# Performance work log

Measured on AMD Instinct MI355X. Metric: run time of the kernel, lower is better.

Reference implementation:

```python
import jax, jax.numpy as jnp
import numpy as np

N, E = 20000, 320000
IN_DIM = OUT_DIM = E_IN = E_OUT = 128
BN_EPS = 1e-5

def _lrelu(x):
    return jnp.where(x >= 0, x, 0.1 * x)

def setup_inputs() -> dict:
    key = jax.random.key(0)
    ks = jax.random.split(key, 12)
    def w(k, shape):
        return jax.random.normal(k, shape, jnp.float32) * (shape[0] ** -0.5)
    return {
        "h": jax.random.normal(ks[0], (N, IN_DIM), jnp.float32),
        "edge_w": jax.random.normal(ks[1], (E, E_IN), jnp.float32),
        "W_node": w(ks[2], (IN_DIM, OUT_DIM)),
        "W_eedge": w(ks[3], (E_IN, E_IN)),
        "W_esf": w(ks[4], (E_IN, 1)),
        "W_fuse": w(ks[5], (2 * OUT_DIM + E_IN, OUT_DIM)),
        "b_fuse": jnp.zeros((OUT_DIM,), jnp.float32),
        "W_attn": w(ks[6], (OUT_DIM, 1)),
        "W_conc": w(ks[7], (2 * OUT_DIM + E_IN, OUT_DIM)),
        "b_conc": jnp.zeros((OUT_DIM,), jnp.float32),
        "bn_gamma": jnp.ones((E_IN,), jnp.float32),
        "bn_beta": jnp.zeros((E_IN,), jnp.float32),
        "W_aggre": w(ks[8], (2 * OUT_DIM + 2 * E_IN, E_OUT)),
        "src": jax.random.randint(ks[9], (E,), 0, N),
        "dst": jax.random.randint(ks[10], (E,), 0, N),
    }

def reference(h, edge_w, W_node, W_eedge, W_esf, W_fuse, b_fuse, W_attn,
              W_conc, b_conc, bn_gamma, bn_beta, W_aggre, src, dst):
    # eval mode: dropout = identity, BatchNorm uses running stats (mean 0, var 1)
    hn = h @ W_node                       # embed_node -> ndata['h'] = ndata['oh']
    # self_attention: ow = embed_edge(w); w = edge_sf_atten(lrelu(ow)) * ow
    ow = edge_w @ W_eedge                 # [E, e_in]
    w1 = (_lrelu(ow) @ W_esf) * ow        # [E, e_in]
    # inter_attention
    hs, hd = hn[src], hn[dst]             # [E, out]
    sat = jnp.concatenate([hs, hd, w1], axis=-1)          # [E, 2*out+e_in]
    inw = _lrelu(sat @ W_fuse + b_fuse)                   # [E, out]
    a = inw @ W_attn                                      # [E, 1]
    w2 = a * w1                                           # edata['w']
    # reduce_func2: segment softmax over incoming edges (grouped by dst)
    s = a[:, 0]
    m = jax.ops.segment_max(s, dst, num_segments=N)
    e = jnp.exp(s - m[dst])
    denom = jax.ops.segment_sum(e, dst, num_segments=N)
    alpha = (e / denom[dst])[:, None]                     # [E, 1]
    t = jnp.concatenate([hs, w2], axis=-1)                # [E, out+e_in]
    h_agg = jax.ops.segment_sum(alpha * t, dst, num_segments=N)  # [N, out+e_in]
    h_new = jnp.concatenate([h_agg, hn], axis=-1) @ W_conc + b_conc
    # DGL only updates nodes that received messages; zero-indegree keep embed_node(h)
    indeg = jax.ops.segment_sum(jnp.ones((E,), jnp.float32), dst, num_segments=N)
    h_out = jnp.where(indeg[:, None] > 0, h_new, hn)      # [N, out]
    # edge_calc: BN(w2) then aggre_embed_edge(cat(src_h, dst_h, bn_w, ow))
    w_bn = (w2 / jnp.sqrt(jnp.float32(1.0) + BN_EPS)) * bn_gamma + bn_beta
    z = jnp.concatenate([h_out[src], h_out[dst], w_bn, ow], axis=-1)
    w_out = z @ W_aggre                                   # [E, e_out]
    return h_out, w_out, sat
```

## Files before the change

### kernel.cpp

```cpp
#include <hip/hip_runtime.h>
#include <hip/hip_bf16.h>

#define TB 256
#define TBM 512
#define BM 64
#define BK 32
#define BN 128
#define ASTR 68
#define MAXD 160

static constexpr int NN = 20000;
static constexpr int NE = 320000;

static constexpr long long OFF_HN   = 0;
static constexpr long long OFF_OW   = 2560000;
static constexpr long long OFF_S    = 43520000;
static constexpr long long OFF_DEN  = 43840000;
static constexpr long long OFF_CUR  = 43860000;
static constexpr long long OFF_HAGG = 43880000;
static constexpr long long OFF_WT   = 49000000;
static constexpr long long WS_FLOATS = 49140000;

static constexpr int U_E = 0;
static constexpr int U_F = 32768;
static constexpr int U_A = 131072;

static constexpr long long OUT_HOUT = 0;
static constexpr long long OUT_WOUT = 2560000;
static constexpr long long OUT_SAT  = 43520000;

typedef __attribute__((ext_vector_type(8))) short s8v;
typedef __attribute__((ext_vector_type(4))) float f32x4;
typedef __attribute__((ext_vector_type(4))) unsigned short u16x4;

#define MFMA16(a,b,c) __builtin_amdgcn_mfma_f32_16x16x32_bf16(a,b,c,0,0,0)

__device__ __forceinline__ float lrelu(float x){ return x >= 0.f ? x : 0.1f*x; }

__device__ __forceinline__ void gl16(const void* g, void* l){
    __builtin_amdgcn_global_load_lds(
        (const __attribute__((address_space(1))) void*)g,
        (__attribute__((address_space(3))) void*)l, 16, 0, 0);
}

__device__ __forceinline__ void split1(float f, unsigned short& hi, unsigned short& lo){
    __hip_bfloat16 h = __float2bfloat16(f);
    float hf = __bfloat162float(h);
    __hip_bfloat16 l = __float2bfloat16(f - hf);
    hi = __builtin_bit_cast(unsigned short, h);
    lo = __builtin_bit_cast(unsigned short, l);
}
__device__ __forceinline__ void split8(float4 a, float4 b, s8v& hi, s8v& lo){
    float v[8] = {a.x,a.y,a.z,a.w,b.x,b.y,b.z,b.w};
#pragma unroll
    for (int j = 0; j < 8; ++j){
        unsigned short hs, ls;
        split1(v[j], hs, ls);
        hi[j] = (short)hs; lo[j] = (short)ls;
    }
}
__device__ __forceinline__ float bfp(unsigned p){
    return __uint_as_float(p & 0xffff0000u) + __uint_as_float(p << 16);
}

__device__ __forceinline__ int lds_a(int row, int g){
    return row*32 + ((g ^ (row & 3)) << 3);
}

__device__ __forceinline__ void store_At(float (*Ast)[ASTR], int k4, int r, float4 v){
    Ast[k4+0][r] = v.x; Ast[k4+1][r] = v.y; Ast[k4+2][r] = v.z; Ast[k4+3][r] = v.w;
}
__device__ __forceinline__ void mm_chunk(const float (*Ast)[ASTR], const float (*Bs)[BN],
                                         int r0, int c0, float acc[4][8]){
#pragma unroll 4
    for (int k = 0; k < BK; ++k){
        const float4 av = *(const float4*)&Ast[k][r0];
        const float4 b0 = *(const float4*)&Bs[k][c0];
        const float4 b1 = *(const float4*)&Bs[k][64 + c0];
        const float a0=av.x, a1=av.y, a2=av.z, a3=av.w;
        const float b[8] = {b0.x,b0.y,b0.z,b0.w,b1.x,b1.y,b1.z,b1.w};
#pragma unroll
        for (int j = 0; j < 8; ++j){
            acc[0][j] = fmaf(a0, b[j], acc[0][j]);
            acc[1][j] = fmaf(a1, b[j], acc[1][j]);
            acc[2][j] = fmaf(a2, b[j], acc[2][j]);
            acc[3][j] = fmaf(a3, b[j], acc[3][j]);
        }
    }
}
__device__ __forceinline__ void load_B(const float* __restrict__ W, int kc,
                                       float (*Bs)[BN], int tid){
#pragma unroll
    for (int p = 0; p < 4; ++p){
        int idx = p*TB + tid;
        int row = idx >> 5;
        int c4  = (idx & 31) << 2;
        *(float4*)&Bs[row][c4] = *(const float4*)&W[(size_t)(kc+row)*BN + c4];
    }
}

__global__ __launch_bounds__(TB) void k_prep(const float* __restrict__ We,
                                             const float* __restrict__ Wf,
                                             const float* __restrict__ Wa,
                                             unsigned short* __restrict__ wt,
                                             int* __restrict__ cur){
    int id = blockIdx.x*TB + threadIdx.x;
    if (id < NN) cur[id] = 0;
    unsigned short hs, ls;
    if (id < 16384){
        int n = id >> 7, k = id & 127;
        split1(We[(size_t)k*128 + n], hs, ls);
        wt[U_E + id] = hs; wt[U_E + 16384 + id] = ls;
    } else if (id < 65536){
        int local = id - 16384;
        int n = local / 384, k = local - n*384;
        split1(Wf[(size_t)k*128 + n], hs, ls);
        wt[U_F + local] = hs; wt[U_F + 49152 + local] = ls;
    } else if (id < 131072){
        int local = id - 65536;
        int n = local >> 9, k = local & 511;
        split1(Wa[(size_t)k*128 + n], hs, ls);
        wt[U_A + local] = hs; wt[U_A + 65536 + local] = ls;
    }
}

__global__ __launch_bounds__(TB) void kB_count(const int* __restrict__ dst,
                                               int* __restrict__ cur){
    int e = blockIdx.x*TB + threadIdx.x;
    atomicAdd(&cur[dst[e]], 1);
}
__global__ __launch_bounds__(TB) void kC_scan(int* __restrict__ cur,
                                              int* __restrict__ offs){
    __shared__ int part[TB];
    __shared__ int spre[TB];
    const int tid = threadIdx.x;
    const int CH = (NN + TB - 1) / TB;
    const int base = tid * CH;
    int sum = 0;
    for (int i = 0; i < CH; ++i){ int idx = base + i; if (idx < NN) sum += cur[idx]; }
    part[tid] = sum;
    __syncthreads();
    if (tid == 0){ int r = 0; for (int i = 0; i < TB; ++i){ spre[i] = r; r += part[i]; } }
    __syncthreads();
    int run = spre[tid];
    for (int i = 0; i < CH; ++i){
        int idx = base + i;
        if (idx < NN){ int c = cur[idx]; offs[idx] = run; cur[idx] = run; run += c; }
    }
}
__global__ __launch_bounds__(TB) void kD_scatter(const int* __restrict__ dst,
                                                 int* __restrict__ cur,
                                                 int* __restrict__ eidx){
    int e = blockIdx.x*TB + threadIdx.x;
    int p = atomicAdd(&cur[dst[e]], 1);
    eidx[p] = e;
}

__global__ __launch_bounds__(TB) void k1_hn(const float* __restrict__ h,
                                            const float* __restrict__ Wn,
                                            unsigned short* __restrict__ hnH,
                                            unsigned short* __restrict__ hnL,
                                            unsigned* __restrict__ hnP){
    __shared__ float Ast[BK][ASTR];
    __shared__ float Bs[BK][BN];
    const int tid = threadIdx.x;
    const int rbase = blockIdx.x * BM;
    const int tc = tid & 15, tr = tid >> 4;
    const int r0 = tr*4, c0 = tc*4;
    float acc[4][8] = {};
    for (int kc = 0; kc < 128; kc += BK){
        __syncthreads();
        {
            int lr = tid >> 3, k4 = (tid & 7) << 2;
#pragma unroll
            for (int p = 0; p < 2; ++p){
                int r = p*32 + lr;
                int rr = rbase + r; if (rr >= NN) rr = NN-1;
                float4 v = *(const float4*)&h[(size_t)rr*128 + kc + k4];
                store_At(Ast, k4, r, v);
            }
        }
        load_B(Wn, kc, Bs, tid);
        __syncthreads();
        mm_chunk(Ast, Bs, r0, c0, acc);
    }
#pragma unroll
    for (int i = 0; i < 4; ++i){
        int rr = rbase + r0 + i;
        if (rr < NN){
            u16x4 h0, l0, h1, l1;
            uint4 p0, p1;
#pragma unroll
            for (int j = 0; j < 4; ++j){
                unsigned short hs, ls;
                split1(acc[i][j], hs, ls);
                h0[j] = hs; l0[j] = ls;
                ((unsigned*)&p0)[j] = ((unsigned)hs << 16) | ls;
                split1(acc[i][4+j], hs, ls);
                h1[j] = hs; l1[j] = ls;
                ((unsigned*)&p1)[j] = ((unsigned)hs << 16) | ls;
            }
            *(u16x4*)&hnH[(size_t)rr*128 + c0] = h0;
            *(u16x4*)&hnL[(size_t)rr*128 + c0] = l0;
            *(u16x4*)&hnH[(size_t)rr*128 + 64 + c0] = h1;
            *(u16x4*)&hnL[(size_t)rr*128 + 64 + c0] = l1;
            *(uint4*)&hnP[(size_t)rr*128 + c0] = p0;
            *(uint4*)&hnP[(size_t)rr*128 + 64 + c0] = p1;
        }
    }
}


__global__ __launch_bounds__(TBM) void k2_mfma(const float* __restrict__ ew,
                                               const unsigned short* __restrict__ wtH,
                                               const unsigned short* __restrict__ wtL,
                                               const float* __restrict__ Wesf,
                                               unsigned short* __restrict__ owH,
                                               unsigned short* __restrict__ owL,
                                               float* __restrict__ sat){
    __shared__ __align__(16) unsigned short Ah[2][4096], Al[2][4096], Bh[2][4096], Bl[2][4096];
    __shared__ float sEsf[128];
    const int tid = threadIdx.x;
    const long long rbase = (long long)blockIdx.x * 128;
    const int lane = tid & 63, w = tid >> 6;
    const int ls = lane & 15, lg = lane >> 4;
    const int srow = tid >> 2, sg = tid & 3;
    const int gsw = sg ^ (srow & 3);
    const int aslot = srow*32 + (gsw << 3);
    if (tid < 128) sEsf[tid] = Wesf[tid];
    f32x4 acc[8] = {};
    auto stage = [&](int nb, int t){
        const int kc = t*32;
        gl16(&wtH[srow*128 + kc + gsw*8], &Bh[nb][w*512]);
        gl16(&wtL[srow*128 + kc + gsw*8], &Bl[nb][w*512]);
        const float* p = &ew[(rbase + srow)*128 + kc + sg*8];
        float4 v0 = *(const float4*)p, v1 = *(const float4*)(p+4);
        s8v hi, lo; split8(v0, v1, hi, lo);
        *(s8v*)&Ah[nb][aslot] = hi; *(s8v*)&Al[nb][aslot] = lo;
    };
    stage(0, 0);
    __syncthreads();
    int cur = 0;
    for (int t = 0; t < 4; ++t){
        if (t+1 < 4) stage(cur^1, t+1);
        s8v ah = *(const s8v*)&Ah[cur][lds_a(w*16 + ls, lg)];
        s8v al = *(const s8v*)&Al[cur][lds_a(w*16 + ls, lg)];
#pragma unroll
        for (int ct = 0; ct < 8; ++ct){
            int c = ct*16 + ls;
            s8v bh = *(const s8v*)&Bh[cur][lds_a(c,lg)];
            s8v bl = *(const s8v*)&Bl[cur][lds_a(c,lg)];
            acc[ct] = MFMA16(ah, bh, acc[ct]);
            acc[ct] = MFMA16(ah, bl, acc[ct]);
            acc[ct] = MFMA16(al, bh, acc[ct]);
        }
        __syncthreads();
        cur ^= 1;
    }
#pragma unroll
    for (int reg = 0; reg < 4; ++reg){
        float p = 0.f;
#pragma unroll
        for (int ct = 0; ct < 8; ++ct)
            p += lrelu(acc[ct][reg]) * sEsf[ct*16 + ls];
#pragma unroll
        for (int m = 1; m < 16; m <<= 1) p += __shfl_xor(p, m);
        long long orow = rbase + w*16 + lg*4 + reg;
#pragma unroll
        for (int ct = 0; ct < 8; ++ct){
            float o = acc[ct][reg];
            int col = ct*16 + ls;
            sat[orow*384 + 256 + col] = p * o;
            unsigned short hs_, ls_; split1(o, hs_, ls_);
            owH[orow*128 + col] = hs_;
            owL[orow*128 + col] = ls_;
        }
    }
}

__global__ __launch_bounds__(TBM) void k3_mfma(const unsigned short* __restrict__ hnH,
                                               const unsigned short* __restrict__ hnL,
                                               const unsigned* __restrict__ hnP,
                                               const unsigned short* __restrict__ wtH,
                                               const unsigned short* __restrict__ wtL,
                                               const float* __restrict__ bf,
                                               const float* __restrict__ Wattn,
                                               const int* __restrict__ src,
                                               const int* __restrict__ dst,
                                               float* __restrict__ sat,
                                               float* __restrict__ s_ws){
    __shared__ __align__(16) unsigned short Ah[2][4096], Al[2][4096], Bh[2][4096], Bl[2][4096];
    __shared__ float sBf[128], sAtt[128];
    __shared__ int sSrc[128], sDst[128];
    const int tid = threadIdx.x;
    const long long rbase = (long long)blockIdx.x * 128;
    const int lane = tid & 63, w = tid >> 6;
    const int ls = lane & 15, lg = lane >> 4;
    const int srow = tid >> 2, sg = tid & 3;
    const int gsw = sg ^ (srow & 3);
    const int aslot = srow*32 + (gsw << 3);
    if (tid < 128){
        sBf[tid] = bf[tid]; sAtt[tid] = Wattn[tid];
        sSrc[tid] = src[rbase + tid]; sDst[tid] = dst[rbase + tid];
    }
    __syncthreads();
    f32x4 acc[8] = {};
    auto stage = [&](int nb, int t){
        const int kc = t*32;
        gl16(&wtH[srow*384 + kc + gsw*8], &Bh[nb][w*512]);
        gl16(&wtL[srow*384 + kc + gsw*8], &Bl[nb][w*512]);
        long long e = rbase + srow;
        if (kc < 256){
            int node = (kc < 128) ? sSrc[srow] : sDst[srow];
            int col0 = kc & 127;
            gl16(&hnH[(size_t)node*128 + col0 + gsw*8], &Ah[nb][w*512]);
            gl16(&hnL[(size_t)node*128 + col0 + gsw*8], &Al[nb][w*512]);
            const unsigned* pp = &hnP[(size_t)node*128 + col0 + sg*8];
            uint4 q0 = *(const uint4*)pp, q1 = *(const uint4*)(pp+4);
            float4 v0 = {bfp(q0.x), bfp(q0.y), bfp(q0.z), bfp(q0.w)};
            float4 v1 = {bfp(q1.x), bfp(q1.y), bfp(q1.z), bfp(q1.w)};
            *(float4*)&sat[e*384 + kc + sg*8] = v0;
            *(float4*)&sat[e*384 + kc + sg*8 + 4] = v1;
        } else {
            const float* p = &sat[e*384 + kc + sg*8];
            float4 v0 = *(const float4*)p, v1 = *(const float4*)(p+4);
            s8v hi, lo; split8(v0, v1, hi, lo);
            *(s8v*)&Ah[nb][aslot] = hi; *(s8v*)&Al[nb][aslot] = lo;
        }
    };
    stage(0, 0);
    __syncthreads();
    int cur = 0;
    for (int t = 0; t < 12; ++t){
        if (t+1 < 12) stage(cur^1, t+1);
        s8v ah = *(const s8v*)&Ah[cur][lds_a(w*16 + ls, lg)];
        s8v al = *(const s8v*)&Al[cur][lds_a(w*16 + ls, lg)];
#pragma unroll
        for (int ct = 0; ct < 8; ++ct){
            int c = ct*16 + ls;
            s8v bh = *(const s8v*)&Bh[cur][lds_a(c,lg)];
            s8v bl = *(const s8v*)&Bl[cur][lds_a(c,lg)];
            acc[ct] = MFMA16(ah, bh, acc[ct]);
            acc[ct] = MFMA16(ah, bl, acc[ct]);
            acc[ct] = MFMA16(al, bh, acc[ct]);
        }
        __syncthreads();
        cur ^= 1;
    }
#pragma unroll
    for (int reg = 0; reg < 4; ++reg){
        float p = 0.f;
#pragma unroll
        for (int ct = 0; ct < 8; ++ct){
            int col = ct*16 + ls;
            p += lrelu(acc[ct][reg] + sBf[col]) * sAtt[col];
        }
#pragma unroll
        for (int m = 1; m < 16; m <<= 1) p += __shfl_xor(p, m);
        if (ls == 0) s_ws[rbase + w*16 + lg*4 + reg] = p;
    }
}

__global__ __launch_bounds__(TB) void k5_agg(const float* __restrict__ s,
                                             const unsigned* __restrict__ hnP,
                                             const float* __restrict__ sat,
                                             const int* __restrict__ src,
                                             const int* __restrict__ eidx,
                                             const int* __restrict__ offs,
                                             const int* __restrict__ cur,
                                             float* __restrict__ hagg,
                                             float* __restrict__ den){
    __shared__ int   sEu[4][MAXD];
    __shared__ int   sEs[4][MAXD];
    __shared__ float sAl[4][MAXD];
    __shared__ float sWc[4][MAXD];
    const int wv = threadIdx.x >> 6, lane = threadIdx.x & 63;
    const int n = blockIdx.x*4 + wv;
    int* Eu = sEu[wv]; int* Es = sEs[wv];
    float* Al = sAl[wv]; float* Wc = sWc[wv];
    const int start = offs[n];
    const int deg = cur[n] - start;
    const int dc = deg < MAXD ? deg : MAXD;
    for (int i = lane; i < dc; i += 64) Eu[i] = eidx[start+i];
    __syncthreads();
    for (int i = lane; i < dc; i += 64){
        int my = Eu[i], r = 0;
        for (int j = 0; j < dc; ++j) r += (Eu[j] < my);
        Es[r] = my;
    }
    __syncthreads();
    float lm = -3.402823466e38f;
    for (int i = lane; i < dc; i += 64){
        int e = Es[i];
        float sv = s[e];
        Wc[i] = sv;
        Eu[i] = src[e];
        lm = fmaxf(lm, sv);
    }
    for (int i = MAXD + lane; i < deg; i += 64) lm = fmaxf(lm, s[eidx[start+i]]);
#pragma unroll
    for (int m2 = 32; m2; m2 >>= 1) lm = fmaxf(lm, __shfl_xor(lm, m2));
    const float m = lm;
    float lsum = 0.f;
    for (int i = lane; i < dc; i += 64){
        float ev = expf(Wc[i] - m);
        Al[i] = ev;
        lsum += ev;
    }
    for (int i = MAXD + lane; i < deg; i += 64) lsum += expf(s[eidx[start+i]] - m);
#pragma unroll
    for (int m2 = 32; m2; m2 >>= 1) lsum += __shfl_xor(lsum, m2);
    const float denom = lsum;
    const float inv = (deg > 0) ? 1.f/denom : 0.f;
    for (int i = lane; i < dc; i += 64){
        float al = Al[i] * inv;
        Al[i] = al;
        Wc[i] = al * Wc[i];
    }
    __syncthreads();
    float a0=0.f, a1=0.f, a2=0.f, a3=0.f;
    for (int i = 0; i < dc; ++i){
        int sI = Eu[i];
        size_t e = (size_t)Es[i];
        float al = Al[i], wc = Wc[i];
        unsigned p0 = hnP[(size_t)sI*128 + lane];
        unsigned p1 = hnP[(size_t)sI*128 + 64 + lane];
        float w0 = sat[e*384 + 256 + lane];
        float w1v = sat[e*384 + 256 + 64 + lane];
        a0 = fmaf(al, bfp(p0), a0);
        a1 = fmaf(al, bfp(p1), a1);
        a2 = fmaf(wc, w0, a2);
        a3 = fmaf(wc, w1v, a3);
    }
    for (int i = MAXD; i < deg; ++i){
        int e = eidx[start+i];
        float sv = s[e];
        float al = expf(sv - m) * inv;
        float wc = al * sv;
        int sI = src[e];
        a0 = fmaf(al, bfp(hnP[(size_t)sI*128 + lane]), a0);
        a1 = fmaf(al, bfp(hnP[(size_t)sI*128 + 64 + lane]), a1);
        a2 = fmaf(wc, sat[(size_t)e*384 + 256 + lane], a2);
        a3 = fmaf(wc, sat[(size_t)e*384 + 256 + 64 + lane], a3);
    }
    const size_t b = (size_t)n*256;
    hagg[b + lane] = a0;
    hagg[b + 64 + lane] = a1;
    hagg[b + 128 + lane] = a2;
    hagg[b + 192 + lane] = a3;
    if (lane == 0) den[n] = (deg > 0) ? denom : 0.f;
}

__global__ __launch_bounds__(TB) void k6_conc(const float* hagg,
                                              const unsigned* __restrict__ hnP,
                                              const float* __restrict__ Wc,
                                              const float* __restrict__ bc,
                                              const float* __restrict__ den,
                                              float* __restrict__ hout,
                                              unsigned short* houtHL){
    __shared__ float Ast[BK][ASTR];
    __shared__ float Bs[BK][BN];
    __shared__ float sBc[BN];
    const int tid = threadIdx.x;
    const int rbase = blockIdx.x * BM;
    const int tc = tid & 15, tr = tid >> 4;
    const int r0 = tr*4, c0 = tc*4;
    if (tid < BN) sBc[tid] = bc[tid];
    float acc[4][8] = {};
    for (int chunk = 0; chunk < 12; ++chunk){
        int kc = chunk * BK;
        __syncthreads();
        {
            int lr = tid >> 3, k4 = (tid & 7) << 2;
#pragma unroll
            for (int p = 0; p < 2; ++p){
                int r = p*32 + lr;
                int rr = rbase + r; if (rr >= NN) rr = NN-1;
                float4 v;
                if (chunk < 8) v = *(const float4*)&hagg[(size_t)rr*256 + kc + k4];
                else {
                    int cb = (kc - 256) + k4;
                    uint4 q = *(const uint4*)&hnP[(size_t)rr*128 + cb];
                    v.x = bfp(q.x); v.y = bfp(q.y); v.z = bfp(q.z); v.w = bfp(q.w);
                }
                store_At(Ast, k4, r, v);
            }
        }
        load_B(Wc, kc, Bs, tid);
        __syncthreads();
        mm_chunk(Ast, Bs, r0, c0, acc);
    }
#pragma unroll
    for (int i = 0; i < 4; ++i){
        int rr = rbase + r0 + i;
        if (rr >= NN) continue;
        bool keep = den[rr] > 0.f;
        float o[8];
#pragma unroll
        for (int j = 0; j < 8; ++j){
            int col = (j < 4) ? (c0 + j) : (60 + c0 + j);
            float fb = bfp(hnP[(size_t)rr*128 + col]);
            o[j] = keep ? acc[i][j] + sBc[col] : fb;
        }
        float4 o0 = {o[0],o[1],o[2],o[3]}, o1 = {o[4],o[5],o[6],o[7]};
        *(float4*)&hout[(size_t)rr*128 + c0] = o0;
        *(float4*)&hout[(size_t)rr*128 + 64 + c0] = o1;
        u16x4 h0, l0, h1, l1;
#pragma unroll
        for (int j = 0; j < 4; ++j){
            unsigned short hs, ls2;
            split1(o[j], hs, ls2);   h0[j] = hs; l0[j] = ls2;
            split1(o[4+j], hs, ls2); h1[j] = hs; l1[j] = ls2;
        }
        *(u16x4*)&houtHL[(size_t)rr*512 + c0] = h0;
        *(u16x4*)&houtHL[(size_t)rr*512 + 128 + c0] = l0;
        *(u16x4*)&houtHL[(size_t)rr*512 + 64 + c0] = h1;
        *(u16x4*)&houtHL[(size_t)rr*512 + 128 + 64 + c0] = l1;
    }
}

__global__ __launch_bounds__(TBM) void k7_mfma(const unsigned short* __restrict__ houtHL,
                                               const unsigned short* __restrict__ owH,
                                               const unsigned short* __restrict__ owL,
                                               const float* __restrict__ sarr,
                                               const float* __restrict__ sat,
                                               const float* __restrict__ gamma,
                                               const float* __restrict__ beta,
                                               const unsigned short* __restrict__ wtH,
                                               const unsigned short* __restrict__ wtL,
                                               const int* __restrict__ src,
                                               const int* __restrict__ dst,
                                               float* __restrict__ w2out){
    __shared__ __align__(16) unsigned short Ah[2][4096], Al[2][4096], Bh[2][4096], Bl[2][4096];
    __shared__ float sGam[128], sBet[128], sS[128];
    __shared__ int sSrc[128], sDst[128];
    const int tid = threadIdx.x;
    const long long rbase = (long long)blockIdx.x * 128;
    const int lane = tid & 63, w = tid >> 6;
    const int ls = lane & 15, lg = lane >> 4;
    const int srow = tid >> 2, sg = tid & 3;
    const int gsw = sg ^ (srow & 3);
    const int aslot = srow*32 + (gsw << 3);
    const float ISR = 0.9999950000374997f;
    if (tid < 128){
        sGam[tid] = gamma[tid] * ISR; sBet[tid] = beta[tid];
        sSrc[tid] = src[rbase + tid]; sDst[tid] = dst[rbase + tid];
        sS[tid] = sarr[rbase + tid];
    }
    __syncthreads();
    f32x4 acc[8] = {};
    auto stage = [&](int nb, int t){
        const int kc = t*32;
        gl16(&wtH[srow*512 + kc + gsw*8], &Bh[nb][w*512]);
        gl16(&wtL[srow*512 + kc + gsw*8], &Bl[nb][w*512]);
        long long e = rbase + srow;
        if (kc < 256){
            int node = (kc < 128) ? sSrc[srow] : sDst[srow];
            int col0 = kc & 127;
            gl16(&houtHL[(size_t)node*512 + col0 + gsw*8], &Ah[nb][w*512]);
            gl16(&houtHL[(size_t)node*512 + 128 + col0 + gsw*8], &Al[nb][w*512]);
        } else if (kc < 384){
            int cb = (kc - 256) + sg*8;
            float se = sS[srow];
            const float* p = &sat[e*384 + 256 + cb];
            float4 v0 = *(const float4*)p, v1 = *(const float4*)(p+4);
            v0.x = fmaf(v0.x*se, sGam[cb+0], sBet[cb+0]);
            v0.y = fmaf(v0.y*se, sGam[cb+1], sBet[cb+1]);
            v0.z = fmaf(v0.z*se, sGam[cb+2], sBet[cb+2]);
            v0.w = fmaf(v0.w*se, sGam[cb+3], sBet[cb+3]);
            v1.x = fmaf(v1.x*se, sGam[cb+4], sBet[cb+4]);
            v1.y = fmaf(v1.y*se, sGam[cb+5], sBet[cb+5]);
            v1.z = fmaf(v1.z*se, sGam[cb+6], sBet[cb+6]);
            v1.w = fmaf(v1.w*se, sGam[cb+7], sBet[cb+7]);
            s8v hi, lo; split8(v0, v1, hi, lo);
            *(s8v*)&Ah[nb][aslot] = hi; *(s8v*)&Al[nb][aslot] = lo;
        } else {
            int col0 = kc - 384;
            gl16(&owH[e*128 + col0 + gsw*8], &Ah[nb][w*512]);
            gl16(&owL[e*128 + col0 + gsw*8], &Al[nb][w*512]);
        }
    };
    stage(0, 0);
    __syncthreads();
    int cur = 0;
    for (int t = 0; t < 16; ++t){
        if (t+1 < 16) stage(cur^1, t+1);
        s8v ah = *(const s8v*)&Ah[cur][lds_a(w*16 + ls, lg)];
        s8v al = *(const s8v*)&Al[cur][lds_a(w*16 + ls, lg)];
#pragma unroll
        for (int ct = 0; ct < 8; ++ct){
            int c = ct*16 + ls;
            s8v bh = *(const s8v*)&Bh[cur][lds_a(c,lg)];
            s8v bl = *(const s8v*)&Bl[cur][lds_a(c,lg)];
            acc[ct] = MFMA16(ah, bh, acc[ct]);
            acc[ct] = MFMA16(ah, bl, acc[ct]);
            acc[ct] = MFMA16(al, bh, acc[ct]);
        }
        __syncthreads();
        cur ^= 1;
    }
#pragma unroll
    for (int reg = 0; reg < 4; ++reg){
        long long orow = rbase + w*16 + lg*4 + reg;
#pragma unroll
        for (int ct = 0; ct < 8; ++ct)
            w2out[orow*128 + ct*16 + ls] = acc[ct][reg];
    }
}

extern "C" void kernel_launch(void* const* d_in, const int* in_sizes, int n_in,
                              void* d_out, int out_size, void* d_ws, size_t ws_size,
                              hipStream_t stream){
    (void)in_sizes; (void)n_in; (void)out_size;
    const float* h       = (const float*)d_in[0];
    const float* edge_w  = (const float*)d_in[1];
    const float* W_node  = (const float*)d_in[2];
    const float* W_eedge = (const float*)d_in[3];
    const float* W_esf   = (const float*)d_in[4];
    const float* W_fuse  = (const float*)d_in[5];
    const float* b_fuse  = (const float*)d_in[6];
    const float* W_attn  = (const float*)d_in[7];
    const float* W_conc  = (const float*)d_in[8];
    const float* b_conc  = (const float*)d_in[9];
    const float* gamma   = (const float*)d_in[10];
    const float* beta    = (const float*)d_in[11];
    const float* W_aggre = (const float*)d_in[12];
    const int*   src     = (const int*)d_in[13];
    const int*   dst     = (const int*)d_in[14];

    float* out    = (float*)d_out;
    float* o_hout = out + OUT_HOUT;
    float* o_wout = out + OUT_WOUT;
    float* o_sat  = out + OUT_SAT;

    if (ws_size < (size_t)WS_FLOATS * 4) return;
    float* ws     = (float*)d_ws;
    unsigned short* w_hnH = (unsigned short*)(ws + OFF_HN);
    unsigned short* w_hnL = w_hnH + (size_t)NN*128;
    unsigned short* w_owH = (unsigned short*)(ws + OFF_OW);
    unsigned short* w_owL = w_owH + (size_t)NE*128;
    float* w_s    = ws + OFF_S;
    float* w_den  = ws + OFF_DEN;
    int*   w_cur  = (int*)(ws + OFF_CUR);
    float* w_hagg = ws + OFF_HAGG;
    unsigned short* w_houtHL = (unsigned short*)w_hagg;
    unsigned short* w_wt = (unsigned short*)(ws + OFF_WT);

    unsigned* w_hnP = (unsigned*)o_wout;
    int* w_eidx = (int*)o_hout;
    int* w_offs = w_eidx + NE;

    hipLaunchKernelGGL(k_prep,    dim3(131072/TB), dim3(TB), 0, stream,
                       W_eedge, W_fuse, W_aggre, w_wt, w_cur);
    hipLaunchKernelGGL(kB_count,  dim3(NE/TB), dim3(TB), 0, stream, dst, w_cur);
    hipLaunchKernelGGL(kC_scan,   dim3(1), dim3(TB), 0, stream, w_cur, w_offs);
    hipLaunchKernelGGL(kD_scatter,dim3(NE/TB), dim3(TB), 0, stream, dst, w_cur, w_eidx);
    hipLaunchKernelGGL(k1_hn,     dim3((NN+BM-1)/BM), dim3(TB), 0, stream, h, W_node,
                       w_hnH, w_hnL, w_hnP);
    hipLaunchKernelGGL(k2_mfma,   dim3(NE/128), dim3(TBM), 0, stream, edge_w,
                       w_wt + U_E, w_wt + U_E + 128*128, W_esf,
                       w_owH, w_owL, o_sat);
    hipLaunchKernelGGL(k3_mfma,   dim3(NE/128), dim3(TBM), 0, stream, w_hnH, w_hnL, w_hnP,
                       w_wt + U_F, w_wt + U_F + 128*384, b_fuse, W_attn,
                       src, dst, o_sat, w_s);
    hipLaunchKernelGGL(k5_agg,    dim3(NN/4), dim3(TB), 0, stream, w_s, w_hnP, o_sat,
                       src, w_eidx, w_offs, w_cur, w_hagg, w_den);
    hipLaunchKernelGGL(k6_conc,   dim3((NN+BM-1)/BM), dim3(TB), 0, stream, w_hagg,
                       w_hnP, W_conc, b_conc, w_den, o_hout, w_houtHL);
    hipLaunchKernelGGL(k7_mfma,   dim3(NE/128), dim3(TBM), 0, stream, w_houtHL,
                       w_owH, w_owL, w_s, o_sat, gamma, beta,
                       w_wt + U_A, w_wt + U_A + 128*512,
                       src, dst, o_wout);
}
```

Baseline: 711.5 us.

## Precompute per-node projections of h_out through W_aggre instead of per-edge GEMM

The h_out[src] and h_out[dst] slices of the final edge GEMM are moved to node level. A new fp32 kernel computes h_out @ W_aggre rows 0..255 for each of the 20000 nodes, and the edge kernel now runs only K=256 (bn_w and ow) with split-bf16 MFMA. It then adds two gathered 128-wide node rows per edge in the epilogue. This halves the K-loop of the dominant edge GEMM and removes the hi/lo split of h_out. The cost is an extra node GEMM and scattered fp32 gathers of the node projections per edge.

```diff
diff --git a/kernel.cpp b/kernel.cpp
--- a/kernel.cpp
+++ b/kernel.cpp
@@ -11,19 +11,23 @@
 
 static constexpr int NN = 20000;
 static constexpr int NE = 320000;
-
-static constexpr long long OFF_HN   = 0;
-static constexpr long long OFF_OW   = 2560000;
-static constexpr long long OFF_S    = 43520000;
-static constexpr long long OFF_DEN  = 43840000;
-static constexpr long long OFF_CUR  = 43860000;
-static constexpr long long OFF_HAGG = 43880000;
-static constexpr long long OFF_WT   = 49000000;
-static constexpr long long WS_FLOATS = 49140000;
-
-static constexpr int U_E = 0;
-static constexpr int U_F = 32768;
-static constexpr int U_A = 131072;
+static constexpr int NB = 313;
+
+static constexpr long long OFF_OW  = 0;
+static constexpr long long OFF_HN  = 40960000;
+static constexpr long long OFF_PQ  = 43520000;
+static constexpr long long OFF_S   = 48640000;
+static constexpr long long OFF_DEN = 48960000;
+static constexpr long long OFF_CUR = 48980000;
+static constexpr long long OFF_WT  = 49000000;
+static constexpr long long WS_FLOATS = 49100000;
+
+static constexpr int U_EH = 0;
+static constexpr int U_EL = 16384;
+static constexpr int U_FH = 32768;
+static constexpr int U_FL = 81920;
+static constexpr int U_AH = 131072;
+static constexpr int U_AL = 163840;
 
 static constexpr long long OUT_HOUT = 0;
 static constexpr long long OUT_WOUT = 2560000;
@@ -31,6 +35,7 @@
 
 typedef __attribute__((ext_vector_type(8))) short s8v;
 typedef __attribute__((ext_vector_type(4))) float f32x4;
+typedef __attribute__((ext_vector_type(8))) unsigned short u16x8;
 typedef __attribute__((ext_vector_type(4))) unsigned short u16x4;
 
 #define MFMA16(a,b,c) __builtin_amdgcn_mfma_f32_16x16x32_bf16(a,b,c,0,0,0)
@@ -110,17 +115,17 @@
     if (id < 16384){
         int n = id >> 7, k = id & 127;
         split1(We[(size_t)k*128 + n], hs, ls);
-        wt[U_E + id] = hs; wt[U_E + 16384 + id] = ls;
+        wt[U_EH + id] = hs; wt[U_EL + id] = ls;
     } else if (id < 65536){
         int local = id - 16384;
         int n = local / 384, k = local - n*384;
         split1(Wf[(size_t)k*128 + n], hs, ls);
-        wt[U_F + local] = hs; wt[U_F + 49152 + local] = ls;
-    } else if (id < 131072){
+        wt[U_FH + local] = hs; wt[U_FL + local] = ls;
+    } else if (id < 98304){
         int local = id - 65536;
-        int n = local >> 9, k = local & 511;
-        split1(Wa[(size_t)k*128 + n], hs, ls);
-        wt[U_A + local] = hs; wt[U_A + 65536 + local] = ls;
+        int n = local >> 8, kk = local & 255;
+        split1(Wa[(size_t)(256+kk)*128 + n], hs, ls);
+        wt[U_AH + local] = hs; wt[U_AL + local] = ls;
     }
 }
 
@@ -451,13 +456,12 @@
     if (lane == 0) den[n] = (deg > 0) ? denom : 0.f;
 }
 
-__global__ __launch_bounds__(TB) void k6_conc(const float* hagg,
+__global__ __launch_bounds__(TB) void k6_conc(const float* __restrict__ hagg,
                                               const unsigned* __restrict__ hnP,
                                               const float* __restrict__ Wc,
                                               const float* __restrict__ bc,
                                               const float* __restrict__ den,
-                                              float* __restrict__ hout,
-                                              unsigned short* houtHL){
+                                              float* __restrict__ hout){
     __shared__ float Ast[BK][ASTR];
     __shared__ float Bs[BK][BN];
     __shared__ float sBc[BN];
@@ -505,32 +509,61 @@
         float4 o0 = {o[0],o[1],o[2],o[3]}, o1 = {o[4],o[5],o[6],o[7]};
         *(float4*)&hout[(size_t)rr*128 + c0] = o0;
         *(float4*)&hout[(size_t)rr*128 + 64 + c0] = o1;
-        u16x4 h0, l0, h1, l1;
-#pragma unroll
-        for (int j = 0; j < 4; ++j){
-            unsigned short hs, ls2;
-            split1(o[j], hs, ls2);   h0[j] = hs; l0[j] = ls2;
-            split1(o[4+j], hs, ls2); h1[j] = hs; l1[j] = ls2;
-        }
-        *(u16x4*)&houtHL[(size_t)rr*512 + c0] = h0;
-        *(u16x4*)&houtHL[(size_t)rr*512 + 128 + c0] = l0;
-        *(u16x4*)&houtHL[(size_t)rr*512 + 64 + c0] = h1;
-        *(u16x4*)&houtHL[(size_t)rr*512 + 128 + 64 + c0] = l1;
-    }
-}
-
-__global__ __launch_bounds__(TBM) void k7_mfma(const unsigned short* __restrict__ houtHL,
-                                               const unsigned short* __restrict__ owH,
-                                               const unsigned short* __restrict__ owL,
-                                               const float* __restrict__ sarr,
-                                               const float* __restrict__ sat,
-                                               const float* __restrict__ gamma,
-                                               const float* __restrict__ beta,
-                                               const unsigned short* __restrict__ wtH,
-                                               const unsigned short* __restrict__ wtL,
-                                               const int* __restrict__ src,
-                                               const int* __restrict__ dst,
-                                               float* __restrict__ w2out){
+    }
+}
+
+__global__ __launch_bounds__(TB) void kNG(const float* __restrict__ aF,
+                                          const float* __restrict__ W,
+                                          float* __restrict__ O){
+    __shared__ float Ast[BK][ASTR];
+    __shared__ float Bs[BK][BN];
+    const int tid = threadIdx.x;
+    const int half = blockIdx.x >= NB ? 1 : 0;
+    const int rbase = (blockIdx.x - half*NB) * BM;
+    const float* Wp = W + (size_t)half*16384;
+    const int tc = tid & 15, tr = tid >> 4;
+    const int r0 = tr*4, c0 = tc*4;
+    float acc[4][8] = {};
+    for (int kc = 0; kc < 128; kc += BK){
+        __syncthreads();
+        {
+            int lr = tid >> 3, k4 = (tid & 7) << 2;
+#pragma unroll
+            for (int p = 0; p < 2; ++p){
+                int r = p*32 + lr;
+                int rr = rbase + r; if (rr >= NN) rr = NN-1;
+                float4 v = *(const float4*)&aF[(size_t)rr*128 + kc + k4];
+                store_At(Ast, k4, r, v);
+            }
+        }
+        load_B(Wp, kc, Bs, tid);
+        __syncthreads();
+        mm_chunk(Ast, Bs, r0, c0, acc);
+    }
+#pragma unroll
+    for (int i = 0; i < 4; ++i){
+        int rr = rbase + r0 + i;
+        if (rr < NN){
+            float4 o0 = {acc[i][0],acc[i][1],acc[i][2],acc[i][3]};
+            float4 o1 = {acc[i][4],acc[i][5],acc[i][6],acc[i][7]};
+            *(float4*)&O[(size_t)rr*256 + half*128 + c0] = o0;
+            *(float4*)&O[(size_t)rr*256 + half*128 + 64 + c0] = o1;
+        }
+    }
+}
+
+__global__ __launch_bounds__(TBM) void k7p(const unsigned short* __restrict__ owH,
+                                           const unsigned short* __restrict__ owL,
+                                           const float* __restrict__ sarr,
+                                           const float* __restrict__ sat,
+                                           const float* __restrict__ Q,
+                                           const float* __restrict__ gamma,
+                                           const float* __restrict__ beta,
+                                           const unsigned short* __restrict__ wtH,
+                                           const unsigned short* __restrict__ wtL,
+                                           const int* __restrict__ src,
+                                           const int* __restrict__ dst,
+                                           float* __restrict__ w2out){
     __shared__ __align__(16) unsigned short Ah[2][4096], Al[2][4096], Bh[2][4096], Bl[2][4096];
     __shared__ float sGam[128], sBet[128], sS[128];
     __shared__ int sSrc[128], sDst[128];
@@ -551,16 +584,11 @@
     f32x4 acc[8] = {};
     auto stage = [&](int nb, int t){
         const int kc = t*32;
-        gl16(&wtH[srow*512 + kc + gsw*8], &Bh[nb][w*512]);
-        gl16(&wtL[srow*512 + kc + gsw*8], &Bl[nb][w*512]);
+        gl16(&wtH[srow*256 + kc + gsw*8], &Bh[nb][w*512]);
+        gl16(&wtL[srow*256 + kc + gsw*8], &Bl[nb][w*512]);
         long long e = rbase + srow;
-        if (kc < 256){
-            int node = (kc < 128) ? sSrc[srow] : sDst[srow];
-            int col0 = kc & 127;
-            gl16(&houtHL[(size_t)node*512 + col0 + gsw*8], &Ah[nb][w*512]);
-            gl16(&houtHL[(size_t)node*512 + 128 + col0 + gsw*8], &Al[nb][w*512]);
-        } else if (kc < 384){
-            int cb = (kc - 256) + sg*8;
+        if (kc < 128){
+            int cb = kc + sg*8;
             float se = sS[srow];
             const float* p = &sat[e*384 + 256 + cb];
             float4 v0 = *(const float4*)p, v1 = *(const float4*)(p+4);
@@ -575,7 +603,7 @@
             s8v hi, lo; split8(v0, v1, hi, lo);
             *(s8v*)&Ah[nb][aslot] = hi; *(s8v*)&Al[nb][aslot] = lo;
         } else {
-            int col0 = kc - 384;
+            int col0 = kc - 128;
             gl16(&owH[e*128 + col0 + gsw*8], &Ah[nb][w*512]);
             gl16(&owL[e*128 + col0 + gsw*8], &Al[nb][w*512]);
         }
@@ -583,15 +611,16 @@
     stage(0, 0);
     __syncthreads();
     int cur = 0;
-    for (int t = 0; t < 16; ++t){
-        if (t+1 < 16) stage(cur^1, t+1);
-        s8v ah = *(const s8v*)&Ah[cur][lds_a(w*16 + ls, lg)];
-        s8v al = *(const s8v*)&Al[cur][lds_a(w*16 + ls, lg)];
+    for (int t = 0; t < 8; ++t){
+        if (t+1 < 8) stage(cur^1, t+1);
+        int r = w*16 + ls;
+        s8v ah = *(const s8v*)&Ah[cur][r*32 + ((lg ^ (r&3)) << 3)];
+        s8v al = *(const s8v*)&Al[cur][r*32 + ((lg ^ (r&3)) << 3)];
 #pragma unroll
         for (int ct = 0; ct < 8; ++ct){
             int c = ct*16 + ls;
-            s8v bh = *(const s8v*)&Bh[cur][lds_a(c,lg)];
-            s8v bl = *(const s8v*)&Bl[cur][lds_a(c,lg)];
+            s8v bh = *(const s8v*)&Bh[cur][c*32 + ((lg ^ (c&3)) << 3)];
+            s8v bl = *(const s8v*)&Bl[cur][c*32 + ((lg ^ (c&3)) << 3)];
             acc[ct] = MFMA16(ah, bh, acc[ct]);
             acc[ct] = MFMA16(ah, bl, acc[ct]);
             acc[ct] = MFMA16(al, bh, acc[ct]);
@@ -601,10 +630,16 @@
     }
 #pragma unroll
     for (int reg = 0; reg < 4; ++reg){
-        long long orow = rbase + w*16 + lg*4 + reg;
-#pragma unroll
-        for (int ct = 0; ct < 8; ++ct)
-            w2out[orow*128 + ct*16 + ls] = acc[ct][reg];
+        int row = w*16 + lg*4 + reg;
+        long long orow = rbase + row;
+        int sI = sSrc[row], dI = sDst[row];
+#pragma unroll
+        for (int ct = 0; ct < 8; ++ct){
+            int col = ct*16 + ls;
+            w2out[orow*128 + col] = acc[ct][reg]
+                                  + Q[(size_t)sI*256 + col]
+                                  + Q[(size_t)dI*256 + 128 + col];
+        }
     }
 }
 
@@ -635,40 +670,38 @@
 
     if (ws_size < (size_t)WS_FLOATS * 4) return;
     float* ws     = (float*)d_ws;
+    unsigned short* w_owH = (unsigned short*)(ws + OFF_OW);
+    unsigned short* w_owL = w_owH + (size_t)NE*128;
     unsigned short* w_hnH = (unsigned short*)(ws + OFF_HN);
     unsigned short* w_hnL = w_hnH + (size_t)NN*128;
-    unsigned short* w_owH = (unsigned short*)(ws + OFF_OW);
-    unsigned short* w_owL = w_owH + (size_t)NE*128;
+    float* w_PQ   = ws + OFF_PQ;
     float* w_s    = ws + OFF_S;
     float* w_den  = ws + OFF_DEN;
     int*   w_cur  = (int*)(ws + OFF_CUR);
-    float* w_hagg = ws + OFF_HAGG;
-    unsigned short* w_houtHL = (unsigned short*)w_hagg;
     unsigned short* w_wt = (unsigned short*)(ws + OFF_WT);
 
     unsigned* w_hnP = (unsigned*)o_wout;
     int* w_eidx = (int*)o_hout;
     int* w_offs = w_eidx + NE;
 
-    hipLaunchKernelGGL(k_prep,    dim3(131072/TB), dim3(TB), 0, stream,
+    hipLaunchKernelGGL(k_prep,    dim3(98304/TB), dim3(TB), 0, stream,
                        W_eedge, W_fuse, W_aggre, w_wt, w_cur);
     hipLaunchKernelGGL(kB_count,  dim3(NE/TB), dim3(TB), 0, stream, dst, w_cur);
     hipLaunchKernelGGL(kC_scan,   dim3(1), dim3(TB), 0, stream, w_cur, w_offs);
     hipLaunchKernelGGL(kD_scatter,dim3(NE/TB), dim3(TB), 0, stream, dst, w_cur, w_eidx);
-    hipLaunchKernelGGL(k1_hn,     dim3((NN+BM-1)/BM), dim3(TB), 0, stream, h, W_node,
+    hipLaunchKernelGGL(k1_hn,     dim3(NB), dim3(TB), 0, stream, h, W_node,
                        w_hnH, w_hnL, w_hnP);
     hipLaunchKernelGGL(k2_mfma,   dim3(NE/128), dim3(TBM), 0, stream, edge_w,
-                       w_wt + U_E, w_wt + U_E + 128*128, W_esf,
-                       w_owH, w_owL, o_sat);
+                       w_wt + U_EH, w_wt + U_EL, W_esf, w_owH, w_owL, o_sat);
     hipLaunchKernelGGL(k3_mfma,   dim3(NE/128), dim3(TBM), 0, stream, w_hnH, w_hnL, w_hnP,
-                       w_wt + U_F, w_wt + U_F + 128*384, b_fuse, W_attn,
+                       w_wt + U_FH, w_wt + U_FL, b_fuse, W_attn,
                        src, dst, o_sat, w_s);
     hipLaunchKernelGGL(k5_agg,    dim3(NN/4), dim3(TB), 0, stream, w_s, w_hnP, o_sat,
-                       src, w_eidx, w_offs, w_cur, w_hagg, w_den);
-    hipLaunchKernelGGL(k6_conc,   dim3((NN+BM-1)/BM), dim3(TB), 0, stream, w_hagg,
-                       w_hnP, W_conc, b_conc, w_den, o_hout, w_houtHL);
-    hipLaunchKernelGGL(k7_mfma,   dim3(NE/128), dim3(TBM), 0, stream, w_houtHL,
-                       w_owH, w_owL, w_s, o_sat, gamma, beta,
-                       w_wt + U_A, w_wt + U_A + 128*512,
-                       src, dst, o_wout);
-}
+                       src, w_eidx, w_offs, w_cur, w_PQ, w_den);
+    hipLaunchKernelGGL(k6_conc,   dim3(NB), dim3(TB), 0, stream, w_PQ,
+                       w_hnP, W_conc, b_conc, w_den, o_hout);
+    hipLaunchKernelGGL(kNG,       dim3(2*NB), dim3(TB), 0, stream, o_hout, W_aggre, w_PQ);
+    hipLaunchKernelGGL(k7p,       dim3(NE/128), dim3(TBM), 0, stream,
+                       w_owH, w_owL, w_s, o_sat, w_PQ, gamma, beta,
+                       w_wt + U_AH, w_wt + U_AL, src, dst, o_wout);
+}
```

Result: slower. 726.1 us (+2.1%).
